# Optimization experiments

Measured on AMD Instinct MI355X. Metric: run time of the kernel, lower is better.

## Reference

```python
import jax, jax.numpy as jnp
import numpy as np

# Module hyperparameters (match init_kwargs)
C = 64      # in_channels
O = 256     # out_channels
K = 3       # filter_size
SUB = 2     # subsampling
SIGMA = 1.0
SCALE = 1.0 / SIGMA ** 2
EPS = 1e-8


def setup_inputs() -> dict:
    key = jax.random.key(0)
    k1, k2 = jax.random.split(key)
    x = jax.random.normal(k1, (32, C, 64, 64), dtype=jnp.float32)
    weight = jax.random.normal(k2, (O, C * K * K), dtype=jnp.float32)
    return {"x": x, "weight": weight}


def reference(x, weight):
    # Faithful to CKNLayer.forward, but expressed as a direct convolution
    # instead of materializing the im2col (unfold) tensor:
    #   unfold -> per-patch L2 norm -> (patches/norm) @ w_norm.T
    # == conv(x, w_norm) / patch_norm,   patch_norm = sqrt(conv(x^2, ones))
    B, _, H, W = x.shape
    pad = K // 2

    # F.normalize(weight, p=2, dim=1): clamp norm at 1e-12
    w_norm = weight / jnp.maximum(
        jnp.linalg.norm(weight, axis=1, keepdims=True), 1e-12
    )
    # torch unfold orders patch features as (c, kh, kw) -> reshape matches
    w4 = w_norm.reshape(O, C, K, K)

    dn = jax.lax.conv_dimension_numbers(x.shape, w4.shape, ('NCHW', 'OIHW', 'NCHW'))
    dots = jax.lax.conv_general_dilated(
        x, w4, window_strides=(1, 1), padding=[(pad, pad), (pad, pad)],
        dimension_numbers=dn)  # [B, O, H, W]

    ones_k = jnp.ones((1, C, K, K), x.dtype)
    sq = jax.lax.conv_general_dilated(
        x * x, ones_k, window_strides=(1, 1), padding=[(pad, pad), (pad, pad)],
        dimension_numbers=dn)  # [B, 1, H, W] = sum of squares per patch
    patch_norm = jnp.sqrt(jnp.maximum(sq, 0.0)) + EPS

    # Gaussian RBF on the unit sphere: exp(scale * (cos_sim - 1))
    out = jnp.exp(SCALE * (dots / patch_norm - 1.0))  # [B, O, H, W]

    # avg_pool2d(kernel=SUB, stride=SUB), H, W divisible by SUB
    out = out.reshape(B, O, H // SUB, SUB, W // SUB, SUB).mean(axis=(3, 5))
    return out
```

## Files before the change

### kernel.cpp

```cpp
#include <hip/hip_runtime.h>
#include <hip/hip_bf16.h>

typedef __attribute__((ext_vector_type(8))) short bf16x8;
typedef __attribute__((ext_vector_type(4))) float f32x4;
typedef __attribute__((ext_vector_type(16))) float f32x16;
typedef __attribute__((ext_vector_type(4))) unsigned u32x4;

__device__ __forceinline__ unsigned bfbits(float v) {
  __hip_bfloat16 h = __float2bfloat16(v);
  return (unsigned)*reinterpret_cast<unsigned short*>(&h);
}

__device__ __forceinline__ void wnorm_one(const float* __restrict__ w,
                                          ushort* __restrict__ wt,
                                          ushort* __restrict__ wt3,
                                          int o, int c) {
  float v[9];
  float ss = 0.f;
  const float* row = w + o * 576 + c * 9;
#pragma unroll
  for (int j = 0; j < 9; ++j) { v[j] = row[j]; ss += v[j] * v[j]; }
#pragma unroll
  for (int off = 32; off > 0; off >>= 1) ss += __shfl_xor(ss, off);
  const float inv = 1.0f / fmaxf(sqrtf(ss), 1e-12f);
  const int g = o >> 5, n = o & 31;
#pragma unroll
  for (int j = 0; j < 9; ++j) {
    const ushort bv = (ushort)bfbits(v[j] * inv);
    wt[o * 576 + j * 64 + c] = bv;
    const int ks = j * 4 + (c >> 4);
    wt3[((ks * 8 + g) * 32 + n) * 16 + (c & 15)] = bv;
  }
}

__global__ void wnorm_kernel(const float* __restrict__ w,
                             ushort* __restrict__ wt,
                             ushort* __restrict__ wt3) {
  wnorm_one(w, wt, wt3, blockIdx.x, threadIdx.x);
}

__global__ __launch_bounds__(256, 8) void xprep_kernel(
    const float* __restrict__ x, ushort* __restrict__ xt,
    float* __restrict__ css, const float* __restrict__ w,
    ushort* __restrict__ wt, ushort* __restrict__ wt3) {
  __shared__ __align__(16) unsigned tile[64 * 33];
  __shared__ __align__(16) float cssp[4 * 64];
  const int t = threadIdx.x;
  if (blockIdx.y == 32) {
    wnorm_one(w, wt, wt3, blockIdx.x * 4 + (t >> 6), t & 63);
    return;
  }
  const int y = blockIdx.x, b = blockIdx.y;
  const int c = t >> 2, m = t & 3;
  const int lane = t & 63, wv = t >> 6;

  const float* src = x + (((size_t)b * 64 + c) * 64 + y) * 64 + m * 4;
  float f[16];
#pragma unroll
  for (int j4 = 0; j4 < 4; ++j4) {
    const f32x4 v = *(const f32x4*)(src + j4 * 16);
#pragma unroll
    for (int k = 0; k < 4; ++k) f[j4 * 4 + k] = v[k];
  }
  float s[16];
#pragma unroll
  for (int j = 0; j < 16; ++j) {
    float v = f[j] * f[j];
    v += __shfl_xor(v, 4);
    v += __shfl_xor(v, 8);
    v += __shfl_xor(v, 16);
    v += __shfl_xor(v, 32);
    s[j] = v;
  }
  if (lane < 4) {
#pragma unroll
    for (int j4 = 0; j4 < 4; ++j4) {
      f32x4 v = {s[j4 * 4], s[j4 * 4 + 1], s[j4 * 4 + 2], s[j4 * 4 + 3]};
      *(f32x4*)(cssp + wv * 64 + j4 * 16 + lane * 4) = v;
    }
  }
  const int parity = c & 1;
  const int c2 = c >> 1;
#pragma unroll
  for (int j = 0; j < 16; ++j) {
    const float pf = __shfl_xor(f[j], 4);
    const bool mine = parity ? (j >= 8) : (j < 8);
    if (mine) {
      const unsigned dw = parity ? (bfbits(pf) | (bfbits(f[j]) << 16))
                                 : (bfbits(f[j]) | (bfbits(pf) << 16));
      const int px = (j >> 2) * 16 + m * 4 + (j & 3);
      tile[px * 33 + c2] = dw;
    }
  }
  __syncthreads();
  {
    const int xr = t >> 2, q = t & 3;
    unsigned d[8];
#pragma unroll
    for (int i = 0; i < 8; ++i) d[i] = tile[xr * 33 + q * 8 + i];
    ushort* dst = xt + (((size_t)b * 64 + y) * 64 + xr) * 64 + q * 16;
    u32x4 v0 = {d[0], d[1], d[2], d[3]};
    u32x4 v1 = {d[4], d[5], d[6], d[7]};
    *(u32x4*)dst = v0;
    *(u32x4*)(dst + 8) = v1;
  }
  if (t < 64) {
    const float sum = cssp[t] + cssp[64 + t] + cssp[128 + t] + cssp[192 + t];
    css[((size_t)b * 64 + y) * 64 + t] = sum;
  }
}

__global__ __launch_bounds__(512, 4) void ckn_main(
    const ushort* __restrict__ xt, const float* __restrict__ css,
    const ushort* __restrict__ wt3, float* __restrict__ out) {
  __shared__ __align__(16) char smem[67328];
  char* const xs = smem;
  float* const pool = (float*)(smem + 33792);
  float* const invp = (float*)(smem + 66816);
  const int PS = 258;

  const int tid = threadIdx.x;
  const int y0 = blockIdx.x;
  const int b = blockIdx.y;

  if (tid < 128) {
    const int ry = tid >> 6, xx = tid & 63;
    const int yc = 2 * y0 + ry;
    float s = 0.f;
#pragma unroll
    for (int dy = -1; dy <= 1; ++dy) {
      const int yy = yc + dy;
      if ((unsigned)yy < 64u) s += css[((size_t)b * 64 + yy) * 64 + xx];
    }
    const float sl = __shfl_up(s, 1);
    const float sr = __shfl_down(s, 1);
    const float tot = s + ((xx > 0) ? sl : 0.f) + ((xx < 63) ? sr : 0.f);
    invp[tid] = 1.0f / (sqrtf(fmaxf(tot, 0.f)) + 1e-8f);
  }

  if (tid < 64) {
    const int r4 = tid >> 4, colsel = (tid >> 3) & 1, cblk = tid & 7;
    *(f32x4*)(xs + r4 * 8448 + colsel * 65 * 128 + cblk * 16) =
        (f32x4){0.f, 0.f, 0.f, 0.f};
  }

  {
    const int xx = tid >> 3;
    const int c0 = 8 * ((tid & 7) ^ ((xx + 1) & 7));
    const ushort* srcb = xt + ((size_t)b * 64) * 4096 + (size_t)xx * 64 + c0;
#pragma unroll
    for (int r4 = 0; r4 < 4; ++r4) {
      const int y_img = 2 * y0 - 1 + r4;
      char* dst = xs + r4 * 8448 + 128 + tid * 16;
      if ((unsigned)y_img < 64u) {
        const ushort* src = srcb + (size_t)y_img * 4096;
        __builtin_amdgcn_global_load_lds(
            (const __attribute__((address_space(1))) void*)src,
            (__attribute__((address_space(3))) void*)dst, 16, 0, 0);
      } else {
        *(f32x4*)dst = (f32x4){0.f, 0.f, 0.f, 0.f};
      }
    }
  }

  const int lane = tid & 63;
  const int wid = tid >> 6;
  const int wave_m = wid & 1;
  const int wave_n = wid >> 1;
  const int lane31 = lane & 31;
  const int hi = lane >> 5;

  const ushort* wb3 = wt3 + (size_t)lane31 * 16 + hi * 8;
  const int g0 = wave_n * 2;

  bf16x8 bq[4][2];
#pragma unroll
  for (int d = 0; d < 4; ++d)
#pragma unroll
    for (int nf = 0; nf < 2; ++nf)
      bq[d][nf] = *(const bf16x8*)(wb3 + (size_t)(d * 8 + g0 + nf) * 512);

  const int hi16 = hi << 4;
  int PH[2][3];
#pragma unroll
  for (int mf = 0; mf < 2; ++mf)
#pragma unroll
    for (int kw = 0; kw < 3; ++kw) {
      const int col = mf * 32 + lane31 + kw;
      PH[mf][kw] = (col * 128 + ((col & 7) << 4)) ^ hi16;
    }
  const int rb0 = wave_m * 8448;

  __syncthreads();

  f32x16 acc[2][2];
#pragma unroll
  for (int i = 0; i < 2; ++i)
#pragma unroll
    for (int j = 0; j < 2; ++j)
#pragma unroll
      for (int e = 0; e < 16; ++e) acc[i][j][e] = 0.f;

#pragma unroll
  for (int ks = 0; ks < 36; ++ks) {
    const int t9 = ks >> 2;
    const int kh = t9 / 3, kw = t9 % 3;
    const int ksc = (ks & 3) << 5;
    const int cur = ks & 3;
    bf16x8 afrag[2];
#pragma unroll
    for (int mf = 0; mf < 2; ++mf)
      afrag[mf] = *(const bf16x8*)(xs + rb0 + kh * 8448 + (PH[mf][kw] ^ ksc));
    __builtin_amdgcn_s_setprio(1);
#pragma unroll
    for (int mf = 0; mf < 2; ++mf)
#pragma unroll
      for (int nf = 0; nf < 2; ++nf)
        acc[mf][nf] = __builtin_amdgcn_mfma_f32_32x32x16_bf16(
            afrag[mf], bq[cur][nf], acc[mf][nf], 0, 0, 0);
    __builtin_amdgcn_s_setprio(0);
    if (ks + 4 < 36) {
#pragma unroll
      for (int nf = 0; nf < 2; ++nf)
        bq[cur][nf] =
            *(const bf16x8*)(wb3 + (size_t)((ks + 4) * 8 + g0 + nf) * 512);
    }
  }

  if (wave_m == 1) {
#pragma unroll
    for (int mf = 0; mf < 2; ++mf)
#pragma unroll
      for (int q = 0; q < 4; ++q) {
        const f32x4 ip = *(const f32x4*)(invp + 64 + mf * 32 + 8 * q + 4 * hi);
        const int px = mf * 16 + 4 * q + 2 * hi;
#pragma unroll
        for (int nf = 0; nf < 2; ++nf) {
          const int o = wave_n * 64 + nf * 32 + lane31;
          const float e0 = __expf(acc[mf][nf][4 * q + 0] * ip[0] - 1.f);
          const float e1 = __expf(acc[mf][nf][4 * q + 1] * ip[1] - 1.f);
          const float e2 = __expf(acc[mf][nf][4 * q + 2] * ip[2] - 1.f);
          const float e3 = __expf(acc[mf][nf][4 * q + 3] * ip[3] - 1.f);
          pool[px * PS + o] = e0 + e1;
          pool[(px + 1) * PS + o] = e2 + e3;
        }
      }
  }
  __syncthreads();
  if (wave_m == 0) {
#pragma unroll
    for (int mf = 0; mf < 2; ++mf)
#pragma unroll
      for (int q = 0; q < 4; ++q) {
        const f32x4 ip = *(const f32x4*)(invp + mf * 32 + 8 * q + 4 * hi);
        const int px = mf * 16 + 4 * q + 2 * hi;
#pragma unroll
        for (int nf = 0; nf < 2; ++nf) {
          const int o = wave_n * 64 + nf * 32 + lane31;
          const float e0 = __expf(acc[mf][nf][4 * q + 0] * ip[0] - 1.f);
          const float e1 = __expf(acc[mf][nf][4 * q + 1] * ip[1] - 1.f);
          const float e2 = __expf(acc[mf][nf][4 * q + 2] * ip[2] - 1.f);
          const float e3 = __expf(acc[mf][nf][4 * q + 3] * ip[3] - 1.f);
          pool[px * PS + o] = 0.25f * (pool[px * PS + o] + e0 + e1);
          pool[(px + 1) * PS + o] = 0.25f * (pool[(px + 1) * PS + o] + e2 + e3);
        }
      }
  }
  __syncthreads();

  const size_t obase = (((size_t)b * 256) * 32 + y0) * 32;
#pragma unroll
  for (int j = 0; j < 4; ++j) {
    const int o = j * 64 + (tid >> 3);
    const int ch = (tid & 7) * 4;
    const f32x4 v = {pool[(ch + 0) * PS + o], pool[(ch + 1) * PS + o],
                     pool[(ch + 2) * PS + o], pool[(ch + 3) * PS + o]};
    *(f32x4*)(out + obase + (size_t)o * 1024 + ch) = v;
  }
}

__global__ __launch_bounds__(512, 4) void ckn_main_v1(
    const float* __restrict__ x, const ushort* __restrict__ wt,
    float* __restrict__ out) {
  __shared__ __align__(16) char smem[43552];
  char* const xs = smem;
  float* const invp = (float*)(smem + 33792);
  float* const cs = (float*)(smem + 34304);
  float* const csp = (float*)(smem + 35360);
  float* const pool = (float*)smem;

  const int tid = threadIdx.x;
  const int y0 = blockIdx.x;
  const int b = blockIdx.y;

  if (tid < 64) {
    const int r4 = tid >> 4, colsel = (tid >> 3) & 1, cblk = tid & 7;
    const int col = colsel * 65;
    *(f32x4*)(xs + r4 * 8448 + col * 128 + cblk * 16) =
        (f32x4){0.f, 0.f, 0.f, 0.f};
  }
  {
    const int xx = tid & 63;
    const int cg = tid >> 6;
    const int col = xx + 1;
    const int sw = (cg * 16) ^ ((col & 7) << 4);
#pragma unroll
    for (int r4 = 0; r4 < 4; ++r4) {
      const int y_img = 2 * y0 - 1 + r4;
      char* dst = xs + r4 * 8448 + col * 128 + sw;
      if ((unsigned)y_img < 64u) {
        const float* src =
            x + (((size_t)b * 64 + cg * 8) * 64 + y_img) * 64 + xx;
        float ss = 0.f;
        union { bf16x8 v; ushort u[8]; } pk;
#pragma unroll
        for (int j = 0; j < 8; ++j) {
          const float f = src[(size_t)j * 4096];
          ss += f * f;
          pk.u[j] = (ushort)bfbits(f);
        }
        *(bf16x8*)dst = pk.v;
        csp[(r4 * 8 + cg) * 64 + xx] = ss;
      } else {
        *(bf16x8*)dst = (bf16x8){0, 0, 0, 0, 0, 0, 0, 0};
        csp[(r4 * 8 + cg) * 64 + xx] = 0.f;
      }
    }
  }
  __syncthreads();
  if (tid < 256) {
    const int r4 = tid >> 6, xc = tid & 63;
    float s = 0.f;
#pragma unroll
    for (int cg = 0; cg < 8; ++cg) s += csp[(r4 * 8 + cg) * 64 + xc];
    cs[r4 * 66 + xc + 1] = s;
  }
  if (tid >= 256 && tid < 264) {
    const int t = tid - 256;
    cs[(t >> 1) * 66 + (t & 1) * 65] = 0.f;
  }
  __syncthreads();
  if (tid < 128) {
    const int ry = tid >> 6, xp = tid & 63;
    float s = 0.f;
#pragma unroll
    for (int dr = 0; dr < 3; ++dr)
#pragma unroll
      for (int dc = 0; dc < 3; ++dc) s += cs[(ry + dr) * 66 + xp + dc];
    invp[tid] = 1.0f / (sqrtf(fmaxf(s, 0.f)) + 1e-8f);
  }
  __syncthreads();

  const int lane = tid & 63;
  const int wid = tid >> 6;
  const int wave_m = wid & 1;
  const int wave_n = wid >> 1;
  const int lane16 = lane & 15;
  const int klane = lane >> 4;
  const int o_base = wave_n * 64;

  f32x4 acc[4][4];
#pragma unroll
  for (int i = 0; i < 4; ++i)
#pragma unroll
    for (int j = 0; j < 4; ++j) acc[i][j] = (f32x4){0.f, 0.f, 0.f, 0.f};
  const ushort* wbase = wt + (o_base + lane16) * 576 + klane * 8;
#pragma unroll
  for (int ks = 0; ks < 18; ++ks) {
    const int t9 = ks >> 1;
    const int kh = t9 / 3, kw = t9 % 3;
    const int cb = (ks & 1) * 64 + klane * 16;
    bf16x8 bfrag[4];
#pragma unroll
    for (int fn = 0; fn < 4; ++fn)
      bfrag[fn] = *(const bf16x8*)(wbase + fn * 16 * 576 + ks * 32);
    const int r4 = wave_m + kh;
#pragma unroll
    for (int fm = 0; fm < 4; ++fm) {
      const int col = fm * 16 + lane16 + kw;
      const int addr = r4 * 8448 + col * 128 + (cb ^ ((col & 7) << 4));
      const bf16x8 afrag = *(const bf16x8*)(xs + addr);
#pragma unroll
      for (int fn = 0; fn < 4; ++fn)
        acc[fm][fn] = __builtin_amdgcn_mfma_f32_16x16x32_bf16(
            afrag, bfrag[fn], acc[fm][fn], 0, 0, 0);
    }
  }
  float ep0[4][4], ep1[4][4];
#pragma unroll
  for (int fm = 0; fm < 4; ++fm) {
    const int m = wave_m * 64 + fm * 16 + klane * 4;
    const f32x4 ip = *(const f32x4*)(invp + m);
#pragma unroll
    for (int fn = 0; fn < 4; ++fn) {
      const f32x4 v = acc[fm][fn];
      const float e0 = __expf(v[0] * ip[0] - 1.f);
      const float e1 = __expf(v[1] * ip[1] - 1.f);
      const float e2 = __expf(v[2] * ip[2] - 1.f);
      const float e3 = __expf(v[3] * ip[3] - 1.f);
      ep0[fm][fn] = e0 + e1;
      ep1[fm][fn] = e2 + e3;
    }
  }
  __syncthreads();
  if (wave_m == 1) {
#pragma unroll
    for (int fm = 0; fm < 4; ++fm) {
      const int ox = fm * 8 + klane * 2;
#pragma unroll
      for (int fn = 0; fn < 4; ++fn) {
        const int o = o_base + fn * 16 + lane16;
        *(float2*)(pool + o * 32 + ox) = make_float2(ep0[fm][fn], ep1[fm][fn]);
      }
    }
  }
  __syncthreads();
  if (wave_m == 0) {
#pragma unroll
    for (int fm = 0; fm < 4; ++fm) {
      const int ox = fm * 8 + klane * 2;
#pragma unroll
      for (int fn = 0; fn < 4; ++fn) {
        const int o = o_base + fn * 16 + lane16;
        const float2 othr = *(const float2*)(pool + o * 32 + ox);
        const float r0 = 0.25f * (ep0[fm][fn] + othr.x);
        const float r1 = 0.25f * (ep1[fm][fn] + othr.y);
        *(float2*)(out + ((((size_t)b * 256 + o) * 32 + y0) * 32 + ox)) =
            make_float2(r0, r1);
      }
    }
  }
}

extern "C" void kernel_launch(void* const* d_in, const int* in_sizes, int n_in,
                              void* d_out, int out_size, void* d_ws,
                              size_t ws_size, hipStream_t stream) {
  const float* x = (const float*)d_in[0];
  const float* w = (const float*)d_in[1];
  float* out = (float*)d_out;

  const size_t XT_BYTES = 32ull * 64 * 64 * 64 * 2;
  const size_t CSS_BYTES = 32ull * 64 * 64 * 4;
  const size_t WT_BYTES = 256ull * 576 * 2;
  const size_t NEED = XT_BYTES + CSS_BYTES + 2 * WT_BYTES;

  if (ws_size >= NEED) {
    ushort* xt = (ushort*)d_ws;
    float* css = (float*)((char*)d_ws + XT_BYTES);
    ushort* wt = (ushort*)((char*)d_ws + XT_BYTES + CSS_BYTES);
    ushort* wt3 = (ushort*)((char*)d_ws + XT_BYTES + CSS_BYTES + WT_BYTES);

    xprep_kernel<<<dim3(64, 33), dim3(256), 0, stream>>>(x, xt, css, w, wt,
                                                         wt3);
    ckn_main<<<dim3(32, 32), dim3(512), 0, stream>>>(xt, css, wt3, out);
  } else {
    ushort* wt = (ushort*)d_ws;
    ushort* wt3 = wt + 256 * 576;
    if (ws_size >= 2 * WT_BYTES) {
      wnorm_kernel<<<dim3(256), dim3(64), 0, stream>>>(w, wt, wt3);
      ckn_main_v1<<<dim3(32, 32), dim3(512), 0, stream>>>(x, wt, out);
    }
  }
}
```

Measured before the change: 78.62 us.

## Split output channels across two blocks and alias pool buffer onto input tile

The main kernel now handles 128 output channels per block instead of 256, with a new grid dimension selecting the channel half. Each wave keeps one accumulator pair instead of two, and the pooling buffer reuses the input tile's shared memory after an added barrier. Shared memory drops by about half and the launch bound asks for 6 blocks per CU, raising occupancy. In exchange the input tile is loaded and the patch norms are computed twice as often, and each wave does half the MFMA work per A fragment, lowering reuse.

```diff
diff --git a/kernel.cpp b/kernel.cpp
--- a/kernel.cpp
+++ b/kernel.cpp
@@ -110,18 +110,19 @@
   }
 }
 
-__global__ __launch_bounds__(512, 4) void ckn_main(
+__global__ __launch_bounds__(512, 6) void ckn_main(
     const ushort* __restrict__ xt, const float* __restrict__ css,
     const ushort* __restrict__ wt3, float* __restrict__ out) {
-  __shared__ __align__(16) char smem[67328];
+  __shared__ __align__(16) char smem[34304];
   char* const xs = smem;
-  float* const pool = (float*)(smem + 33792);
-  float* const invp = (float*)(smem + 66816);
-  const int PS = 258;
+  float* const pool = (float*)smem;
+  float* const invp = (float*)(smem + 33792);
+  const int PS = 130;
 
   const int tid = threadIdx.x;
   const int y0 = blockIdx.x;
-  const int b = blockIdx.y;
+  const int nh = blockIdx.y;
+  const int b = blockIdx.z;
 
   if (tid < 128) {
     const int ry = tid >> 6, xx = tid & 63;
@@ -169,16 +170,14 @@
   const int wave_n = wid >> 1;
   const int lane31 = lane & 31;
   const int hi = lane >> 5;
-
-  const ushort* wb3 = wt3 + (size_t)lane31 * 16 + hi * 8;
-  const int g0 = wave_n * 2;
-
-  bf16x8 bq[4][2];
+  const int g = nh * 4 + wave_n;
+
+  const ushort* wb3 = wt3 + (size_t)g * 512 + lane31 * 16 + hi * 8;
+
+  bf16x8 bq[4];
 #pragma unroll
   for (int d = 0; d < 4; ++d)
-#pragma unroll
-    for (int nf = 0; nf < 2; ++nf)
-      bq[d][nf] = *(const bf16x8*)(wb3 + (size_t)(d * 8 + g0 + nf) * 512);
+    bq[d] = *(const bf16x8*)(wb3 + (size_t)d * 4096);
 
   const int hi16 = hi << 4;
   int PH[2][3];
@@ -193,13 +192,11 @@
 
   __syncthreads();
 
-  f32x16 acc[2][2];
+  f32x16 acc[2];
 #pragma unroll
   for (int i = 0; i < 2; ++i)
 #pragma unroll
-    for (int j = 0; j < 2; ++j)
-#pragma unroll
-      for (int e = 0; e < 16; ++e) acc[i][j][e] = 0.f;
+    for (int e = 0; e < 16; ++e) acc[i][e] = 0.f;
 
 #pragma unroll
   for (int ks = 0; ks < 36; ++ks) {
@@ -214,19 +211,14 @@
     __builtin_amdgcn_s_setprio(1);
 #pragma unroll
     for (int mf = 0; mf < 2; ++mf)
-#pragma unroll
-      for (int nf = 0; nf < 2; ++nf)
-        acc[mf][nf] = __builtin_amdgcn_mfma_f32_32x32x16_bf16(
-            afrag[mf], bq[cur][nf], acc[mf][nf], 0, 0, 0);
+      acc[mf] = __builtin_amdgcn_mfma_f32_32x32x16_bf16(afrag[mf], bq[cur],
+                                                        acc[mf], 0, 0, 0);
     __builtin_amdgcn_s_setprio(0);
-    if (ks + 4 < 36) {
-#pragma unroll
-      for (int nf = 0; nf < 2; ++nf)
-        bq[cur][nf] =
-            *(const bf16x8*)(wb3 + (size_t)((ks + 4) * 8 + g0 + nf) * 512);
-    }
-  }
-
+    if (ks + 4 < 36)
+      bq[cur] = *(const bf16x8*)(wb3 + (size_t)(ks + 4) * 4096);
+  }
+
+  __syncthreads();
   if (wave_m == 1) {
 #pragma unroll
     for (int mf = 0; mf < 2; ++mf)
@@ -234,16 +226,13 @@
       for (int q = 0; q < 4; ++q) {
         const f32x4 ip = *(const f32x4*)(invp + 64 + mf * 32 + 8 * q + 4 * hi);
         const int px = mf * 16 + 4 * q + 2 * hi;
-#pragma unroll
-        for (int nf = 0; nf < 2; ++nf) {
-          const int o = wave_n * 64 + nf * 32 + lane31;
-          const float e0 = __expf(acc[mf][nf][4 * q + 0] * ip[0] - 1.f);
-          const float e1 = __expf(acc[mf][nf][4 * q + 1] * ip[1] - 1.f);
-          const float e2 = __expf(acc[mf][nf][4 * q + 2] * ip[2] - 1.f);
-          const float e3 = __expf(acc[mf][nf][4 * q + 3] * ip[3] - 1.f);
-          pool[px * PS + o] = e0 + e1;
-          pool[(px + 1) * PS + o] = e2 + e3;
-        }
+        const int o = wave_n * 32 + lane31;
+        const float e0 = __expf(acc[mf][4 * q + 0] * ip[0] - 1.f);
+        const float e1 = __expf(acc[mf][4 * q + 1] * ip[1] - 1.f);
+        const float e2 = __expf(acc[mf][4 * q + 2] * ip[2] - 1.f);
+        const float e3 = __expf(acc[mf][4 * q + 3] * ip[3] - 1.f);
+        pool[px * PS + o] = e0 + e1;
+        pool[(px + 1) * PS + o] = e2 + e3;
       }
   }
   __syncthreads();
@@ -254,23 +243,20 @@
       for (int q = 0; q < 4; ++q) {
         const f32x4 ip = *(const f32x4*)(invp + mf * 32 + 8 * q + 4 * hi);
         const int px = mf * 16 + 4 * q + 2 * hi;
-#pragma unroll
-        for (int nf = 0; nf < 2; ++nf) {
-          const int o = wave_n * 64 + nf * 32 + lane31;
-          const float e0 = __expf(acc[mf][nf][4 * q + 0] * ip[0] - 1.f);
-          const float e1 = __expf(acc[mf][nf][4 * q + 1] * ip[1] - 1.f);
-          const float e2 = __expf(acc[mf][nf][4 * q + 2] * ip[2] - 1.f);
-          const float e3 = __expf(acc[mf][nf][4 * q + 3] * ip[3] - 1.f);
-          pool[px * PS + o] = 0.25f * (pool[px * PS + o] + e0 + e1);
-          pool[(px + 1) * PS + o] = 0.25f * (pool[(px + 1) * PS + o] + e2 + e3);
-        }
-      }
-  }
-  __syncthreads();
-
-  const size_t obase = (((size_t)b * 256) * 32 + y0) * 32;
-#pragma unroll
-  for (int j = 0; j < 4; ++j) {
+        const int o = wave_n * 32 + lane31;
+        const float e0 = __expf(acc[mf][4 * q + 0] * ip[0] - 1.f);
+        const float e1 = __expf(acc[mf][4 * q + 1] * ip[1] - 1.f);
+        const float e2 = __expf(acc[mf][4 * q + 2] * ip[2] - 1.f);
+        const float e3 = __expf(acc[mf][4 * q + 3] * ip[3] - 1.f);
+        pool[px * PS + o] = 0.25f * (pool[px * PS + o] + e0 + e1);
+        pool[(px + 1) * PS + o] = 0.25f * (pool[(px + 1) * PS + o] + e2 + e3);
+      }
+  }
+  __syncthreads();
+
+  const size_t obase = (((size_t)b * 256 + nh * 128)) * 1024 + y0 * 32;
+#pragma unroll
+  for (int j = 0; j < 2; ++j) {
     const int o = j * 64 + (tid >> 3);
     const int ch = (tid & 7) * 4;
     const f32x4 v = {pool[(ch + 0) * PS + o], pool[(ch + 1) * PS + o],
@@ -452,7 +438,7 @@
 
     xprep_kernel<<<dim3(64, 33), dim3(256), 0, stream>>>(x, xt, css, w, wt,
                                                          wt3);
-    ckn_main<<<dim3(32, 32), dim3(512), 0, stream>>>(xt, css, wt3, out);
+    ckn_main<<<dim3(32, 2, 32), dim3(512), 0, stream>>>(xt, css, wt3, out);
   } else {
     ushort* wt = (ushort*)d_ws;
     ushort* wt3 = wt + 256 * 576;
```

Measured after the change: 76.13 us. 1.03x faster.
